# Kernel tuning notes

Measured on AMD Instinct MI355X. Metric: run time of the kernel, lower is better.

The kernel has to match this reference:

```python
import jax, jax.numpy as jnp
import numpy as np

H = 768   # config.hidden_size
B = 1024  # batch
S = 256   # attention context length
C1, C2, C3 = 202, 183, 11  # num_class for crit, law, time


def setup_inputs() -> dict:
    key = jax.random.key(0)
    ks = jax.random.split(key, 18)
    sd = 1.0 / np.sqrt(H)
    def u(k, shape):
        return jax.random.uniform(k, shape, jnp.float32, -sd, sd)
    return {
        "x": jax.random.normal(ks[0], (B, H), jnp.float32),
        "attn": jax.random.normal(ks[1], (B, S, H), jnp.float32),
        # 3 LSTMCells (tasks crit, law, time), stacked
        "Wih": u(ks[2], (3, 4 * H, H)),
        "Whh": u(ks[3], (3, 4 * H, H)),
        "bih": u(ks[4], (3, 4 * H)),
        "bhh": u(ks[5], (3, 4 * H)),
        # edge (2->3) hidden/cell state Linear (only edge whose FC is reached)
        "hfc_W": u(ks[6], (H, H)), "hfc_b": u(ks[7], (H,)),
        "cfc_W": u(ks[8], (H, H)), "cfc_b": u(ks[9], (H,)),
        # midfc per task
        "midfc_W": u(ks[10], (3, H, H)), "midfc_b": u(ks[11], (3, H)),
        # outfc per task (distinct class counts)
        "out1_W": u(ks[12], (C1, H)), "out1_b": u(ks[13], (C1,)),
        "out2_W": u(ks[14], (C2, H)), "out2_b": u(ks[15], (C2,)),
        "out3_W": u(ks[16], (C3, H)), "out3_b": u(ks[17], (C3,)),
    }


def _lstm_cell(x, h, c, Wih, Whh, bih, bhh):
    # torch nn.LSTMCell: gate order i, f, g, o
    gates = x @ Wih.T + bih + h @ Whh.T + bhh
    i, f, g, o = jnp.split(gates, 4, axis=-1)
    c_new = jax.nn.sigmoid(f) * c + jax.nn.sigmoid(i) * jnp.tanh(g)
    h_new = jax.nn.sigmoid(o) * jnp.tanh(c_new)
    return h_new, c_new


def _attend(h, attn):
    # Attention: ratio = softmax(bmm(attn, h)); result = bmm(attn^T, ratio)
    w = jax.nn.softmax(jnp.einsum('bsh,bh->bs', attn, h), axis=1)
    return jnp.einsum('bsh,bs->bh', attn, w)


def _head(h, mW, mb, oW, ob):
    # more_fc=True: outfc(relu(midfc(h)))
    return jax.nn.relu(h @ mW.T + mb) @ oW.T + ob


def reference(x, attn, Wih, Whh, bih, bhh, hfc_W, hfc_b, cfc_W, cfc_b,
              midfc_W, midfc_b, out1_W, out1_b, out2_W, out2_b, out3_W, out3_b):
    # graph "[(1 2),(1 3),(2 3)]": edges 1->2, 1->3, 2->3; initial hidden_list all zero.
    z = jnp.zeros_like(x)
    # task 1 (crit): runs on zero state; first-touch sets hidden[2]=hidden[3]=(h1,c1)
    h1, c1 = _lstm_cell(x, z, z, Wih[0], Whh[0], bih[0], bhh[0])
    # task 2 (law): state = (h1, c1)
    h2, c2 = _lstm_cell(x, h1, c1, Wih[1], Whh[1], bih[1], bhh[1])
    # edge 2->3 applies the per-edge Linear and accumulates into hidden[3]
    hp3 = h1 + h2 @ hfc_W.T + hfc_b
    cp3 = c1 + c2 @ cfc_W.T + cfc_b
    # task 3 (time)
    h3, c3 = _lstm_cell(x, hp3, cp3, Wih[2], Whh[2], bih[2], bhh[2])
    # attention over encoder context, per task head
    a1 = _attend(h1, attn)
    a2 = _attend(h2, attn)
    a3 = _attend(h3, attn)
    o1 = _head(a1, midfc_W[0], midfc_b[0], out1_W, out1_b)
    o2 = _head(a2, midfc_W[1], midfc_b[1], out2_W, out2_b)
    o3 = _head(a3, midfc_W[2], midfc_b[2], out3_W, out3_b)
    return (o1, o2, o3)
```

## Files before the change

kernel.cpp:

```cpp
#include <hip/hip_runtime.h>


typedef unsigned short u16;
typedef _Float16       f16x8 __attribute__((ext_vector_type(8)));
typedef float          f32x4 __attribute__((ext_vector_type(4)));

#define SWZ(r) ((((r) + ((r) >> 2))) & 3)
#define VMCNT(N) asm volatile("s_waitcnt vmcnt(" #N ")" ::: "memory")
#define KBAR()  do { __builtin_amdgcn_s_barrier(); __builtin_amdgcn_sched_barrier(0); } while (0)

__device__ __forceinline__ u16 f2h(float f) {
  _Float16 h = (_Float16)f;
  return __builtin_bit_cast(u16, h);
}
__device__ __forceinline__ float h2f_(u16 v) {
  return (float)__builtin_bit_cast(_Float16, v);
}
__device__ __forceinline__ float sigm(float x) { return 1.f / (1.f + __expf(-x)); }
__device__ __forceinline__ float ftanh(float x) { return 1.f - 2.f / (__expf(2.f * x) + 1.f); }

__device__ __forceinline__ void gld16(const u16* g, u16* l) {
  __builtin_amdgcn_global_load_lds(
      (const __attribute__((address_space(1))) unsigned int*)(g),
      (__attribute__((address_space(3))) unsigned int*)(l),
      16, 0, 0);
}

struct KP64 { const u16 *pA, *pW; };

__device__ __forceinline__ void stage64(const KP64& kp, int kt,
                                        u16* Asb, u16* Bsb, int wv) {
  const int off = kt * 32;
  gld16(kp.pA + off, Asb + wv * 512);
  gld16(kp.pW + off, Bsb + wv * 512);
}

__device__ __forceinline__ void compute64(const u16* Asb, const u16* Bsb,
                                          int wv, int frow, int fsl, f32x4* acc) {
  const int ar = wv * 16 + frow;
  f16x8 ah = *(const f16x8*)(Asb + ar * 32 + ((fsl ^ SWZ(ar)) * 8));
  f16x8 bh[4];
#pragma unroll
  for (int n = 0; n < 4; ++n) {
    const int br = n * 16 + frow;
    bh[n] = *(const f16x8*)(Bsb + br * 32 + ((fsl ^ SWZ(br)) * 8));
  }
#pragma unroll
  for (int n = 0; n < 4; ++n)
    acc[n] = __builtin_amdgcn_mfma_f32_16x16x32_f16(ah, bh[n], acc[n], 0, 0, 0);
}

__device__ __forceinline__ void kloop64(const KP64& kp, int NT, u16* As, u16* Bs,
                                        int wv, int frow, int fsl, f32x4* acc) {
  stage64(kp, 0, As,        Bs,        wv);
  stage64(kp, 1, As + 2048, Bs + 2048, wv);
  stage64(kp, 2, As + 4096, Bs + 4096, wv);
  for (int t = 0; t < NT - 2; ++t) {
    VMCNT(4); KBAR();
    const int cb = t & 3;
    compute64(As + cb * 2048, Bs + cb * 2048, wv, frow, fsl, acc);
    if (t + 3 < NT) {
      const int sb = (t + 3) & 3;
      stage64(kp, t + 3, As + sb * 2048, Bs + sb * 2048, wv);
    }
  }
  VMCNT(2); KBAR();
  compute64(As + ((NT - 2) & 3) * 2048, Bs + ((NT - 2) & 3) * 2048,
            wv, frow, fsl, acc);
  VMCNT(0); KBAR();
  compute64(As + ((NT - 1) & 3) * 2048, Bs + ((NT - 1) & 3) * 2048,
            wv, frow, fsl, acc);
}

struct GJob {
  const u16* A; const u16* W;
  float* outf; u16* outh;
  const float* bias; const float* bias2; const float* addend;
  int N; int ldc; int relu;
};

__device__ __forceinline__ void run_gemm64(const GJob& jb, int bx, int by,
                                           u16* As, u16* Bs, int tid) {
  const int bn0 = bx * 64;
  if (bn0 >= jb.N) return;
  const int bm0 = by * 64;
  const int lane = tid & 63, wv = tid >> 6;
  const int frow = lane & 15, fsl = lane >> 4;

  const int ra = tid >> 2, csa = (tid & 3) ^ SWZ(ra);
  int wr = bn0 + ra; if (wr >= jb.N) wr = jb.N - 1;

  KP64 kp;
  kp.pA = jb.A + (size_t)(bm0 + ra) * 768 + csa * 8;
  kp.pW = jb.W + (size_t)wr * 768 + csa * 8;

  f32x4 acc[4];
#pragma unroll
  for (int n = 0; n < 4; ++n) acc[n] = (f32x4){0.f, 0.f, 0.f, 0.f};

  kloop64(kp, 24, As, Bs, wv, frow, fsl, acc);

  const int rb = (lane >> 4) * 4;
  const int cc = lane & 15;
#pragma unroll
  for (int n = 0; n < 4; ++n) {
    const int col = bn0 + n * 16 + cc;
    if (col >= jb.N) continue;
    float bv = 0.f;
    if (jb.bias)  bv += jb.bias[col];
    if (jb.bias2) bv += jb.bias2[col];
    const int row0 = bm0 + wv * 16 + rb;
#pragma unroll
    for (int r = 0; r < 4; ++r) {
      const int row = row0 + r;
      float v = acc[n][r] + bv;
      if (jb.addend) v += jb.addend[(size_t)row * jb.ldc + col];
      if (jb.relu)   v = fmaxf(v, 0.f);
      if (jb.outf)   jb.outf[(size_t)row * jb.ldc + col] = v;
      if (jb.outh)   jb.outh[(size_t)row * jb.ldc + col] = f2h(v);
    }
  }
}

__device__ __forceinline__ void run_cell64(const u16* A, const u16* W,
                                           const float* bi, const float* bh_,
                                           const u16* addend,
                                           const float* cprev,
                                           float* hf, float* cf, u16* hh, u16* ch,
                                           int bx, int by,
                                           u16* As, u16* Bs, int tid) {
  const int bj0 = bx * 16;
  const int bm0 = by * 64;
  const int lane = tid & 63, wv = tid >> 6;
  const int frow = lane & 15, fsl = lane >> 4;

  const int ra = tid >> 2, csa = (tid & 3) ^ SWZ(ra);
  const int wr = (ra >> 4) * 768 + bj0 + (ra & 15);

  KP64 kp;
  kp.pA = A + (size_t)(bm0 + ra) * 768 + csa * 8;
  kp.pW = W + (size_t)wr * 768 + csa * 8;

  f32x4 acc[4];
#pragma unroll
  for (int n = 0; n < 4; ++n) acc[n] = (f32x4){0.f, 0.f, 0.f, 0.f};

  kloop64(kp, 24, As, Bs, wv, frow, fsl, acc);

  const int rb = (lane >> 4) * 4;
  const int cc = lane & 15;
  const int j = bj0 + cc;
  float b_i = 0.f, b_f = 0.f, b_g = 0.f, b_o = 0.f;
  if (bi) {
    b_i = bi[j]        + bh_[j];
    b_f = bi[768 + j]  + bh_[768 + j];
    b_g = bi[1536 + j] + bh_[1536 + j];
    b_o = bi[2304 + j] + bh_[2304 + j];
  }
  const int row0 = bm0 + wv * 16 + rb;
#pragma unroll
  for (int r = 0; r < 4; ++r) {
    const int row = row0 + r;
    float gi = acc[0][r] + b_i;
    float gf = acc[1][r] + b_f;
    float gg = acc[2][r] + b_g;
    float go = acc[3][r] + b_o;
    if (addend) {
      const u16* ad = addend + (size_t)row * 6144;
      gi += h2f_(ad[j]); gf += h2f_(ad[768 + j]);
      gg += h2f_(ad[1536 + j]); go += h2f_(ad[2304 + j]);
    }
    float c = sigm(gi) * ftanh(gg);
    if (cprev) c += sigm(gf) * cprev[row * 768 + j];
    float h = sigm(go) * ftanh(c);
    if (hf) hf[row * 768 + j] = h;
    if (cf) cf[row * 768 + j] = c;
    if (hh) hh[row * 768 + j] = f2h(h);
    if (ch) ch[row * 768 + j] = f2h(c);
  }
}

__device__ __forceinline__ void cvt_seg(const float* s, u16* d, int n4,
                                        int gtid, int nthr) {
  for (int i = gtid; i < n4; i += nthr) {
    float4 v = ((const float4*)s)[i];
    ushort4 h;
    h.x = f2h(v.x); h.y = f2h(v.y); h.z = f2h(v.z); h.w = f2h(v.w);
    ((ushort4*)d)[i] = h;
  }
}

__global__ __launch_bounds__(256)
void cvt0_k(const float* x, u16* xh, const float* Wih, u16* Wihh)
{
  const int g = blockIdx.x * 256 + threadIdx.x, N = 2048 * 256;
  cvt_seg(x,   xh,   196608,  g, N);
  cvt_seg(Wih, Wihh, 1769472, g, N);
}

struct K1P {
  const u16 *xh, *Wihh;
  const float *bih, *bhh;
  float *h1f, *c1f; u16* h1h;
  u16* Gpre;
  const float *Whh, *hfcW, *cfcW, *midW, *o1W, *o2W, *o3W;
  u16 *Whhh, *hfch, *cfch, *midh, *o1h, *o2h, *o3h;
};

__global__ __launch_bounds__(256)
void k1_k(K1P p)
{
  __shared__ __align__(16) u16 As[8192];
  __shared__ __align__(16) u16 Bs[8192];
  const int blk = blockIdx.x, tid = threadIdx.x;

  if (blk < 768) {
    run_cell64(p.xh, p.Wihh, p.bih, p.bhh, nullptr, nullptr,
               p.h1f, p.c1f, p.h1h, nullptr, blk % 48, blk / 48, As, Bs, tid);
  } else if (blk < 1536) {
    const int r = blk - 768;
    GJob jb = { p.xh, p.Wihh + (size_t)3072 * 768, nullptr, p.Gpre,
                p.bih + 3072, p.bhh + 3072, nullptr, 3072, 6144, 0 };
    run_gemm64(jb, r % 48, r / 48, As, Bs, tid);
  } else {
    const int g = (blk - 1536) * 256 + tid, N = 384 * 256;
    cvt_seg(p.Whh + 2359296, p.Whhh, 1179648, g, N);
    cvt_seg(p.hfcW, p.hfch, 147456, g, N);
    cvt_seg(p.cfcW, p.cfch, 147456, g, N);
    cvt_seg(p.midW, p.midh, 442368, g, N);
    cvt_seg(p.o1W,  p.o1h,  38784,  g, N);
    cvt_seg(p.o2W,  p.o2h,  35136,  g, N);
    cvt_seg(p.o3W,  p.o3h,  2112,   g, N);
  }
}

struct K2P {
  const u16 *h1h, *Whhh, *xh, *Wihh;
  const u16 *Gpre_t2;
  const float *c1f, *bih, *bhh;
  float *h2f; u16 *Gpre_t3, *h2h, *c2h;
};

__global__ __launch_bounds__(256)
void k2_k(K2P p)
{
  __shared__ __align__(16) u16 As[8192];
  __shared__ __align__(16) u16 Bs[8192];
  const int blk = blockIdx.x, tid = threadIdx.x;

  if (blk < 768) {
    run_cell64(p.h1h, p.Whhh, nullptr, nullptr, p.Gpre_t2, p.c1f,
               p.h2f, nullptr, p.h2h, p.c2h, blk % 48, blk / 48, As, Bs, tid);
  } else {
    const int r = blk - 768;
    GJob jb = { p.xh, p.Wihh + (size_t)6144 * 768, nullptr, p.Gpre_t3,
                p.bih + 6144, p.bhh + 6144, nullptr, 3072, 6144, 0 };
    run_gemm64(jb, r % 48, r / 48, As, Bs, tid);
  }
}

__global__ __launch_bounds__(256)
void cell3_k(const u16* __restrict__ A, const u16* __restrict__ W,
             const u16* __restrict__ addend, const float* __restrict__ cprev,
             float* hf)
{
  __shared__ __align__(16) u16 As[8192];
  __shared__ __align__(16) u16 Bs[8192];
  run_cell64(A, W, nullptr, nullptr, addend, cprev, hf, nullptr, nullptr, nullptr,
             blockIdx.x, blockIdx.y, As, Bs, threadIdx.x);
}

struct GArgs { GJob j[3]; };

__global__ __launch_bounds__(256)
void gemm64_k(GArgs P)
{
  __shared__ __align__(16) u16 As[8192];
  __shared__ __align__(16) u16 Bs[8192];
  run_gemm64(P.j[blockIdx.z], blockIdx.x, blockIdx.y, As, Bs, threadIdx.x);
}

__global__ __launch_bounds__(256, 4)
void attn_k(const float* __restrict__ attn,
            const float* __restrict__ h1, const float* __restrict__ h2,
            const float* __restrict__ h3,
            u16* __restrict__ a1, u16* __restrict__ a2, u16* __restrict__ a3)
{
  const int b = blockIdx.x, tid = threadIdx.x;
  const int lane = tid & 63, wv = tid >> 6;
  __shared__ float accW[4][3][768];
  __shared__ float lsumW[4][3];

  const float* ab = attn + (size_t)b * 196608;
  const int cb = lane * 4;

  float4 hh[3][3];
#pragma unroll
  for (int j = 0; j < 3; ++j) {
    hh[0][j] = *(const float4*)(h1 + b * 768 + j * 256 + cb);
    hh[1][j] = *(const float4*)(h2 + b * 768 + j * 256 + cb);
    hh[2][j] = *(const float4*)(h3 + b * 768 + j * 256 + cb);
  }

  float4 acc[3][3];
#pragma unroll
  for (int t3 = 0; t3 < 3; ++t3)
#pragma unroll
    for (int j = 0; j < 3; ++j) acc[t3][j] = (float4){0.f, 0.f, 0.f, 0.f};
  float lsum[3] = {0.f, 0.f, 0.f};

  const int row0 = wv * 64;
  for (int sub = 0; sub < 32; ++sub) {
    const float* rp = ab + (size_t)(row0 + sub * 2) * 768 + cb;
    float4 vv[2][3];
#pragma unroll
    for (int s = 0; s < 2; ++s)
#pragma unroll
      for (int j = 0; j < 3; ++j)
        vv[s][j] = *(const float4*)(rp + s * 768 + j * 256);

    float q[3][2];
#pragma unroll
    for (int t3 = 0; t3 < 3; ++t3)
#pragma unroll
      for (int s = 0; s < 2; ++s) {
        float d = 0.f;
#pragma unroll
        for (int j = 0; j < 3; ++j) {
          d = fmaf(vv[s][j].x, hh[t3][j].x, d);
          d = fmaf(vv[s][j].y, hh[t3][j].y, d);
          d = fmaf(vv[s][j].z, hh[t3][j].z, d);
          d = fmaf(vv[s][j].w, hh[t3][j].w, d);
        }
        q[t3][s] = d;
      }
#pragma unroll
    for (int t3 = 0; t3 < 3; ++t3)
#pragma unroll
      for (int s = 0; s < 2; ++s) {
#pragma unroll
        for (int d = 1; d < 64; d <<= 1)
          q[t3][s] += __shfl_xor(q[t3][s], d);
        q[t3][s] = __expf(q[t3][s]);
      }
#pragma unroll
    for (int t3 = 0; t3 < 3; ++t3)
#pragma unroll
      for (int s = 0; s < 2; ++s) {
        const float pw = q[t3][s];
        lsum[t3] += pw;
#pragma unroll
        for (int j = 0; j < 3; ++j) {
          acc[t3][j].x = fmaf(pw, vv[s][j].x, acc[t3][j].x);
          acc[t3][j].y = fmaf(pw, vv[s][j].y, acc[t3][j].y);
          acc[t3][j].z = fmaf(pw, vv[s][j].z, acc[t3][j].z);
          acc[t3][j].w = fmaf(pw, vv[s][j].w, acc[t3][j].w);
        }
      }
  }

#pragma unroll
  for (int t3 = 0; t3 < 3; ++t3)
#pragma unroll
    for (int j = 0; j < 3; ++j)
      *(float4*)(&accW[wv][t3][j * 256 + cb]) = acc[t3][j];
  if (lane == 0) {
#pragma unroll
    for (int t3 = 0; t3 < 3; ++t3) lsumW[wv][t3] = lsum[t3];
  }
  __syncthreads();

  float ltot[3];
#pragma unroll
  for (int t3 = 0; t3 < 3; ++t3)
    ltot[t3] = lsumW[0][t3] + lsumW[1][t3] + lsumW[2][t3] + lsumW[3][t3];
  u16* outs[3] = { a1, a2, a3 };
#pragma unroll
  for (int cc = 0; cc < 3; ++cc) {
    const int c = tid + cc * 256;
#pragma unroll
    for (int t3 = 0; t3 < 3; ++t3) {
      float s = accW[0][t3][c] + accW[1][t3][c] + accW[2][t3][c] + accW[3][t3][c];
      outs[t3][b * 768 + c] = f2h(s / ltot[t3]);
    }
  }
}

extern "C" void kernel_launch(void* const* d_in, const int* in_sizes, int n_in,
                              void* d_out, int out_size, void* d_ws, size_t ws_size,
                              hipStream_t stream)
{
  const float* x    = (const float*)d_in[0];
  const float* attn = (const float*)d_in[1];
  const float* Wih  = (const float*)d_in[2];
  const float* Whh  = (const float*)d_in[3];
  const float* bih  = (const float*)d_in[4];
  const float* bhh  = (const float*)d_in[5];
  const float* hfcW = (const float*)d_in[6];
  const float* hfcb = (const float*)d_in[7];
  const float* cfcW = (const float*)d_in[8];
  const float* cfcb = (const float*)d_in[9];
  const float* midW = (const float*)d_in[10];
  const float* midb = (const float*)d_in[11];
  const float* o1W  = (const float*)d_in[12];
  const float* o1b  = (const float*)d_in[13];
  const float* o2W  = (const float*)d_in[14];
  const float* o2b  = (const float*)d_in[15];
  const float* o3W  = (const float*)d_in[16];
  const float* o3b  = (const float*)d_in[17];
  float* out = (float*)d_out;
  char*  ws  = (char*)d_ws;

  u16*   Gpreh = (u16*)(ws + 0);
  float* h1f  = (float*)(ws + 25165824);
  float* c1f  = (float*)(ws + 28311552);
  float* h2f  = (float*)(ws + 31457280);
  float* cp3f = (float*)(ws + 34603008);
  float* h3f  = (float*)(ws + 37748736);
  u16*   xh   = (u16*)(ws + 40894464);
  u16*   Wihh = (u16*)(ws + 42467328);
  u16*   Whhh = (u16*)(ws + 56623104);
  u16*   hfch = (u16*)(ws + 66060288);
  u16*   cfch = (u16*)(ws + 67239936);
  u16*   midh = (u16*)(ws + 68419584);
  u16*   o1h  = (u16*)(ws + 71958528);
  u16*   o2h  = (u16*)(ws + 72268800);
  u16*   o3h  = (u16*)(ws + 72549888);
  u16*   h1h  = (u16*)(ws + 72566784);
  u16*   h2h  = (u16*)(ws + 74139648);
  u16*   c2h  = (u16*)(ws + 75712512);
  u16*   hp3h = (u16*)(ws + 77285376);
  u16*   a1h  = (u16*)(ws + 78858240);
  u16*   a2h  = (u16*)(ws + 80431104);
  u16*   a3h  = (u16*)(ws + 82003968);
  u16*   m1h  = (u16*)(ws + 83576832);
  u16*   m2h  = (u16*)(ws + 85149696);
  u16*   m3h  = (u16*)(ws + 86722560);

  cvt0_k<<<2048, 256, 0, stream>>>(x, xh, Wih, Wihh);

  K1P p1;
  p1.xh = xh; p1.Wihh = Wihh; p1.bih = bih; p1.bhh = bhh;
  p1.h1f = h1f; p1.c1f = c1f; p1.h1h = h1h; p1.Gpre = Gpreh;
  p1.Whh = Whh; p1.hfcW = hfcW; p1.cfcW = cfcW; p1.midW = midW;
  p1.o1W = o1W; p1.o2W = o2W; p1.o3W = o3W;
  p1.Whhh = Whhh; p1.hfch = hfch; p1.cfch = cfch; p1.midh = midh;
  p1.o1h = o1h; p1.o2h = o2h; p1.o3h = o3h;
  k1_k<<<1920, 256, 0, stream>>>(p1);

  K2P p2;
  p2.h1h = h1h; p2.Whhh = Whhh; p2.xh = xh; p2.Wihh = Wihh;
  p2.Gpre_t2 = Gpreh; p2.c1f = c1f; p2.bih = bih; p2.bhh = bhh;
  p2.h2f = h2f; p2.Gpre_t3 = Gpreh + 3072; p2.h2h = h2h; p2.c2h = c2h;
  k2_k<<<1536, 256, 0, stream>>>(p2);

  GArgs P;
  P = GArgs{};
  P.j[0] = { h2h, hfch, nullptr, hp3h, hfcb, nullptr, h1f, 768, 768, 0 };
  P.j[1] = { c2h, cfch, cp3f, nullptr, cfcb, nullptr, c1f, 768, 768, 0 };
  P.j[2] = P.j[1];
  gemm64_k<<<dim3(12, 16, 2), 256, 0, stream>>>(P);

  cell3_k<<<dim3(48, 16), 256, 0, stream>>>(hp3h, Whhh + 2359296,
                                            Gpreh + 3072, cp3f, h3f);

  attn_k<<<1024, 256, 0, stream>>>(attn, h1f, h2f, h3f, a1h, a2h, a3h);

  P = GArgs{};
  P.j[0] = { a1h, midh,           nullptr, m1h, midb,        nullptr, nullptr, 768, 768, 1 };
  P.j[1] = { a2h, midh +  589824, nullptr, m2h, midb +  768, nullptr, nullptr, 768, 768, 1 };
  P.j[2] = { a3h, midh + 1179648, nullptr, m3h, midb + 1536, nullptr, nullptr, 768, 768, 1 };
  gemm64_k<<<dim3(12, 16, 3), 256, 0, stream>>>(P);

  P = GArgs{};
  P.j[0] = { m1h, o1h, out,          nullptr, o1b, nullptr, nullptr, 202, 202, 0 };
  P.j[1] = { m2h, o2h, out + 206848, nullptr, o2b, nullptr, nullptr, 183, 183, 0 };
  P.j[2] = { m3h, o3h, out + 394240, nullptr, o3b, nullptr, nullptr,  11,  11, 0 };
  gemm64_k<<<dim3(4, 16, 3), 256, 0, stream>>>(P);

  (void)in_sizes; (void)n_in; (void)out_size; (void)ws_size;
}
```

Before: 294.3 us.

## Rebalance task-3 input GEMM across k2 and the edge-FC kernel

Half of the task-3 input-projection GEMM tiles are moved out of the k2 kernel into a new k3 kernel, where they run alongside the hfc/cfc edge GEMMs. This replaces the separate gemm64 launch for those edge GEMMs. The aim is to balance the two launches so the small edge GEMM kernel no longer underfills the GPU and k2 gets shorter. The cost is an extra dependency layout, and k3 could end up with a longer tail.

```diff
diff --git a/kernel.cpp b/kernel.cpp
--- a/kernel.cpp
+++ b/kernel.cpp
@@ -255,7 +255,37 @@
     const int r = blk - 768;
     GJob jb = { p.xh, p.Wihh + (size_t)6144 * 768, nullptr, p.Gpre_t3,
                 p.bih + 6144, p.bhh + 6144, nullptr, 3072, 6144, 0 };
-    run_gemm64(jb, r % 48, r / 48, As, Bs, tid);
+    run_gemm64(jb, r % 24, r / 24, As, Bs, tid);
+  }
+}
+
+struct K3P {
+  const u16 *h2h, *hfch, *c2h, *cfch, *xh, *Wihh;
+  const float *hfcb, *cfcb, *h1f, *c1f, *bih, *bhh;
+  float* cp3f; u16 *hp3h, *Gpre_t3;
+};
+
+__global__ __launch_bounds__(256)
+void k3_k(K3P p)
+{
+  __shared__ __align__(16) u16 As[8192];
+  __shared__ __align__(16) u16 Bs[8192];
+  const int blk = blockIdx.x, tid = threadIdx.x;
+
+  if (blk < 192) {
+    GJob jb = { p.h2h, p.hfch, nullptr, p.hp3h, p.hfcb, nullptr, p.h1f,
+                768, 768, 0 };
+    run_gemm64(jb, blk % 12, blk / 12, As, Bs, tid);
+  } else if (blk < 384) {
+    const int r = blk - 192;
+    GJob jb = { p.c2h, p.cfch, p.cp3f, nullptr, p.cfcb, nullptr, p.c1f,
+                768, 768, 0 };
+    run_gemm64(jb, r % 12, r / 12, As, Bs, tid);
+  } else {
+    const int r = blk - 384;
+    GJob jb = { p.xh, p.Wihh + (size_t)6144 * 768, nullptr, p.Gpre_t3,
+                p.bih + 6144, p.bhh + 6144, nullptr, 3072, 6144, 0 };
+    run_gemm64(jb, 24 + r % 24, r / 24, As, Bs, tid);
   }
 }
 
@@ -452,20 +482,22 @@
   p2.h1h = h1h; p2.Whhh = Whhh; p2.xh = xh; p2.Wihh = Wihh;
   p2.Gpre_t2 = Gpreh; p2.c1f = c1f; p2.bih = bih; p2.bhh = bhh;
   p2.h2f = h2f; p2.Gpre_t3 = Gpreh + 3072; p2.h2h = h2h; p2.c2h = c2h;
-  k2_k<<<1536, 256, 0, stream>>>(p2);
-
-  GArgs P;
-  P = GArgs{};
-  P.j[0] = { h2h, hfch, nullptr, hp3h, hfcb, nullptr, h1f, 768, 768, 0 };
-  P.j[1] = { c2h, cfch, cp3f, nullptr, cfcb, nullptr, c1f, 768, 768, 0 };
-  P.j[2] = P.j[1];
-  gemm64_k<<<dim3(12, 16, 2), 256, 0, stream>>>(P);
+  k2_k<<<1152, 256, 0, stream>>>(p2);
+
+  K3P p3;
+  p3.h2h = h2h; p3.hfch = hfch; p3.c2h = c2h; p3.cfch = cfch;
+  p3.xh = xh; p3.Wihh = Wihh;
+  p3.hfcb = hfcb; p3.cfcb = cfcb; p3.h1f = h1f; p3.c1f = c1f;
+  p3.bih = bih; p3.bhh = bhh;
+  p3.cp3f = cp3f; p3.hp3h = hp3h; p3.Gpre_t3 = Gpreh + 3072;
+  k3_k<<<768, 256, 0, stream>>>(p3);
 
   cell3_k<<<dim3(48, 16), 256, 0, stream>>>(hp3h, Whhh + 2359296,
                                             Gpreh + 3072, cp3f, h3f);
 
   attn_k<<<1024, 256, 0, stream>>>(attn, h1f, h2f, h3f, a1h, a2h, a3h);
 
+  GArgs P;
   P = GArgs{};
   P.j[0] = { a1h, midh,           nullptr, m1h, midb,        nullptr, nullptr, 768, 768, 1 };
   P.j[1] = { a2h, midh +  589824, nullptr, m2h, midb +  768, nullptr, nullptr, 768, 768, 1 };
```

New measurement: 293.5 us. No clear change (-0.2%).
